# Performance work log

Hardware: AMD Instinct MI355X
Metric: run time of the kernel (lower is better)

Reference implementation:

```python
import jax, jax.numpy as jnp
import numpy as np

N = 1_000_000   # samples
D_IN = 100      # covariate dim (cfg_density[0][0])
H = 64          # hidden dim
NUM_HEADS = 5   # t-bins [0,.2,.4,.6,.8,1.0]


def setup_inputs() -> dict:
    key = jax.random.key(0)
    ks = jax.random.split(key, 17)
    s = 0.05  # param scale for numerical stability (torch init is data-independent anyway)
    return {
        "t": jax.random.uniform(ks[0], (N,), dtype=jnp.float32),
        "x": jax.random.normal(ks[1], (N, D_IN), dtype=jnp.float32),
        # density feature MLP (two Linear+ReLU layers)
        "dW1": jax.random.normal(ks[2], (D_IN, H), dtype=jnp.float32) * s,
        "db1": jax.random.normal(ks[3], (H,), dtype=jnp.float32) * s,
        "dW2": jax.random.normal(ks[4], (H, H), dtype=jnp.float32) * s,
        "db2": jax.random.normal(ks[5], (H,), dtype=jnp.float32) * s,
        # 5 multi-head branches, each 3 Treat_Linear layers (istreat=1 since isenhance=1)
        "hw1": jax.random.normal(ks[6], (NUM_HEADS, H, H), dtype=jnp.float32) * s,
        "htw1": jax.random.normal(ks[7], (NUM_HEADS, H), dtype=jnp.float32) * s,
        "hb1": jax.random.normal(ks[8], (NUM_HEADS, H), dtype=jnp.float32) * s,
        "hw2": jax.random.normal(ks[9], (NUM_HEADS, H, H), dtype=jnp.float32) * s,
        "htw2": jax.random.normal(ks[10], (NUM_HEADS, H), dtype=jnp.float32) * s,
        "hb2": jax.random.normal(ks[11], (NUM_HEADS, H), dtype=jnp.float32) * s,
        "hw3": jax.random.normal(ks[12], (NUM_HEADS, H, 1), dtype=jnp.float32) * s,
        "htw3": jax.random.normal(ks[13], (NUM_HEADS, 1), dtype=jnp.float32) * s,
        "hb3": jax.random.normal(ks[14], (NUM_HEADS, 1), dtype=jnp.float32) * s,
    }


def reference(t, x, dW1, db1, dW2, db2,
              hw1, htw1, hb1, hw2, htw2, hb2, hw3, htw3, hb3):
    # hidden_features: Linear+ReLU, Linear+ReLU
    h = jax.nn.relu(x @ dW1 + db1)        # [N, H]
    h = jax.nn.relu(h @ dW2 + db2)        # [N, H]

    tt = t[:, None]                        # treatment column [N, 1]
    # bin index per row: t in [0.2*q, 0.2*(q+1)); last bin closed at 1.0
    bins = jnp.clip(jnp.floor(t * NUM_HEADS).astype(jnp.int32), 0, NUM_HEADS - 1)

    out = jnp.zeros((x.shape[0], 1), dtype=h.dtype)
    for q in range(NUM_HEADS):  # fixed small set of structurally-distinct heads
        # Treat_Linear layer 1: feat@W + t*tw + b, relu
        a = jax.nn.relu(h @ hw1[q] + tt * htw1[q] + hb1[q])
        # Treat_Linear layer 2
        a = jax.nn.relu(a @ hw2[q] + tt * htw2[q] + hb2[q])
        # last layer: no activation, islastlayer=1
        a = a @ hw3[q] + tt * htw3[q] + hb3[q]   # [N, 1]
        out = out + jnp.where((bins == q)[:, None], a, 0.0)
    return out  # Drnet returns (None, Q); g is None so we return Q
```

## Files before the change

kernel.cpp:

```cpp
#include <hip/hip_runtime.h>

typedef _Float16 f16;
typedef _Float16 f16x8 __attribute__((ext_vector_type(8)));
typedef float f32x16 __attribute__((ext_vector_type(16)));

#define NB 5
#define DIN 100
#define NT 512
#define GRID 256
#define NWAVES (GRID * 8)

#define FID_W2 14
#define FID_HD 22
#define NFID   (FID_HD + NB * 16)
#define NENT   (NFID * 64)

__global__ __launch_bounds__(256)
void prepack_kernel(const float* __restrict__ dW1, const float* __restrict__ dW2,
                    const float* __restrict__ hw1, const float* __restrict__ hw2,
                    f16x8* __restrict__ pw)
{
    int E = blockIdx.x * 256 + threadIdx.x;
    if (E >= NENT) return;
    int lane = E & 63, fid = E >> 6;
    const float* src; int ks, mt, kmax;
    if (fid < FID_W2)      { int f = fid;          ks = f >> 1; mt = f & 1; src = dW1; kmax = 100; }
    else if (fid < FID_HD) { int f = fid - FID_W2; ks = f >> 1; mt = f & 1; src = dW2; kmax = 64; }
    else {
        int f = fid - FID_HD; int q = f >> 4; int r = f & 15;
        int layer = r >> 3; int rr = r & 7; ks = rr >> 1; mt = rr & 1;
        src = (layer ? hw2 : hw1) + q * 4096; kmax = 64;
    }
    f16x8 v;
    #pragma unroll
    for (int e = 0; e < 8; ++e) {
        int k = 16 * ks + 8 * (lane >> 5) + e;
        int m = 32 * mt + (lane & 31);
        v[e] = (k < kmax) ? (f16)src[k * 64 + m] : (f16)0.f;
    }
    pw[E] = v;
}

__device__ __forceinline__ f32x16 mfma32(f16x8 a, f16x8 b, f32x16 c) {
    return __builtin_amdgcn_mfma_f32_32x32x16_f16(a, b, c, 0, 0, 0);
}
__device__ __forceinline__ f32x16 vzero() {
    f32x16 z;
    #pragma unroll
    for (int i = 0; i < 16; ++i) z[i] = 0.f;
    return z;
}
__device__ __forceinline__ unsigned pk2(float a, float b) {
    union { f16 h[2]; unsigned u; } z; z.h[0] = (f16)a; z.h[1] = (f16)b; return z.u;
}
__device__ __forceinline__ f16x8 frag4(unsigned a, unsigned b, unsigned c, unsigned d) {
    union { unsigned u[4]; f16x8 v; } z; z.u[0]=a; z.u[1]=b; z.u[2]=c; z.u[3]=d; return z.v;
}

#define EPI8T(W, A, BIAS, TW, RT, OFF) { \
    const float4* bp_ = (const float4*)((BIAS) + (OFF)); \
    const float4* tp_ = (const float4*)((TW) + (OFF)); \
    float4 b0_=bp_[0], b1_=bp_[2], b2_=bp_[4], b3_=bp_[6]; \
    float4 t0_=tp_[0], t1_=tp_[2], t2_=tp_[4], t3_=tp_[6]; \
    W[0]=pk2(fmaxf(A[0]+b0_.x+(RT)*t0_.x,0.f), fmaxf(A[1]+b0_.y+(RT)*t0_.y,0.f)); \
    W[1]=pk2(fmaxf(A[2]+b0_.z+(RT)*t0_.z,0.f), fmaxf(A[3]+b0_.w+(RT)*t0_.w,0.f)); \
    W[2]=pk2(fmaxf(A[4]+b1_.x+(RT)*t1_.x,0.f), fmaxf(A[5]+b1_.y+(RT)*t1_.y,0.f)); \
    W[3]=pk2(fmaxf(A[6]+b1_.z+(RT)*t1_.z,0.f), fmaxf(A[7]+b1_.w+(RT)*t1_.w,0.f)); \
    W[4]=pk2(fmaxf(A[8]+b2_.x+(RT)*t2_.x,0.f), fmaxf(A[9]+b2_.y+(RT)*t2_.y,0.f)); \
    W[5]=pk2(fmaxf(A[10]+b2_.z+(RT)*t2_.z,0.f), fmaxf(A[11]+b2_.w+(RT)*t2_.w,0.f)); \
    W[6]=pk2(fmaxf(A[12]+b3_.x+(RT)*t3_.x,0.f), fmaxf(A[13]+b3_.y+(RT)*t3_.y,0.f)); \
    W[7]=pk2(fmaxf(A[14]+b3_.z+(RT)*t3_.z,0.f), fmaxf(A[15]+b3_.w+(RT)*t3_.w,0.f)); }

#define EPI8B(W, A, BIAS, OFF) { \
    const float4* bp_ = (const float4*)((BIAS) + (OFF)); \
    float4 b0_=bp_[0], b1_=bp_[2], b2_=bp_[4], b3_=bp_[6]; \
    W[0]=pk2(fmaxf(A[0]+b0_.x,0.f), fmaxf(A[1]+b0_.y,0.f)); \
    W[1]=pk2(fmaxf(A[2]+b0_.z,0.f), fmaxf(A[3]+b0_.w,0.f)); \
    W[2]=pk2(fmaxf(A[4]+b1_.x,0.f), fmaxf(A[5]+b1_.y,0.f)); \
    W[3]=pk2(fmaxf(A[6]+b1_.z,0.f), fmaxf(A[7]+b1_.w,0.f)); \
    W[4]=pk2(fmaxf(A[8]+b2_.x,0.f), fmaxf(A[9]+b2_.y,0.f)); \
    W[5]=pk2(fmaxf(A[10]+b2_.z,0.f), fmaxf(A[11]+b2_.w,0.f)); \
    W[6]=pk2(fmaxf(A[12]+b3_.x,0.f), fmaxf(A[13]+b3_.y,0.f)); \
    W[7]=pk2(fmaxf(A[14]+b3_.z,0.f), fmaxf(A[15]+b3_.w,0.f)); }

#define MKB(dst, Wm, jb) { \
    unsigned s0_=__shfl_xor(Wm[jb+0],32,64), s1_=__shfl_xor(Wm[jb+1],32,64); \
    unsigned s2_=__shfl_xor(Wm[jb+2],32,64), s3_=__shfl_xor(Wm[jb+3],32,64); \
    dst = frag4(lo ? Wm[jb+0] : s2_, lo ? Wm[jb+1] : s3_, \
                lo ? s0_ : Wm[jb+2], lo ? s1_ : Wm[jb+3]); }

#define ACC16(P, A, B2, T2, W3, RT, OFF) { \
    const float4* bb_=(const float4*)((B2)+(OFF)); const float4* tt_=(const float4*)((T2)+(OFF)); \
    const float4* ww_=(const float4*)((W3)+(OFF)); \
    float4 b0_=bb_[0],b1_=bb_[2],b2_=bb_[4],b3_=bb_[6]; \
    float4 t0_=tt_[0],t1_=tt_[2],t2_=tt_[4],t3_=tt_[6]; \
    float4 w0_=ww_[0],w1_=ww_[2],w2_=ww_[4],w3_=ww_[6]; \
    P += fmaxf(A[0]+b0_.x+(RT)*t0_.x,0.f)*w0_.x + fmaxf(A[1]+b0_.y+(RT)*t0_.y,0.f)*w0_.y \
       + fmaxf(A[2]+b0_.z+(RT)*t0_.z,0.f)*w0_.z + fmaxf(A[3]+b0_.w+(RT)*t0_.w,0.f)*w0_.w \
       + fmaxf(A[4]+b1_.x+(RT)*t1_.x,0.f)*w1_.x + fmaxf(A[5]+b1_.y+(RT)*t1_.y,0.f)*w1_.y \
       + fmaxf(A[6]+b1_.z+(RT)*t1_.z,0.f)*w1_.z + fmaxf(A[7]+b1_.w+(RT)*t1_.w,0.f)*w1_.w \
       + fmaxf(A[8]+b2_.x+(RT)*t2_.x,0.f)*w2_.x + fmaxf(A[9]+b2_.y+(RT)*t2_.y,0.f)*w2_.y \
       + fmaxf(A[10]+b2_.z+(RT)*t2_.z,0.f)*w2_.z + fmaxf(A[11]+b2_.w+(RT)*t2_.w,0.f)*w2_.w \
       + fmaxf(A[12]+b3_.x+(RT)*t3_.x,0.f)*w3_.x + fmaxf(A[13]+b3_.y+(RT)*t3_.y,0.f)*w3_.y \
       + fmaxf(A[14]+b3_.z+(RT)*t3_.z,0.f)*w3_.z + fmaxf(A[15]+b3_.w+(RT)*t3_.w,0.f)*w3_.w; }

__global__ __launch_bounds__(NT, 2)
void drnet_main(const float* __restrict__ t, const float* __restrict__ x,
                const float* __restrict__ db1, const float* __restrict__ db2,
                const float* __restrict__ hb1, const float* __restrict__ htw1,
                const float* __restrict__ hb2, const float* __restrict__ htw2,
                const float* __restrict__ hw3, const float* __restrict__ htw3,
                const float* __restrict__ hb3,
                const f16x8* __restrict__ pw,
                float* __restrict__ out, int N, int NG)
{
    __shared__ __align__(16) f16x8 swts[NENT];
    __shared__ __align__(16) float sb1f[64], sb2f[64];
    __shared__ __align__(16) float shb1[NB*64], shw1t[NB*64], shb2[NB*64], shw2t[NB*64], sw3f[NB*64];
    __shared__ float shtw3[NB], shb3[NB];
    __shared__ unsigned short ssrt[8][64];
    __shared__ float sstv[8][64];
    __shared__ float sout[8][64];

    const int tid = threadIdx.x;
    const int lane = tid & 63;
    const int wv = tid >> 6;
    const int hi = lane >> 5;
    const int sm = lane & 31;
    const bool lo = (hi == 0);

    for (int p = tid; p < 64; p += NT) { sb1f[p] = db1[p]; sb2f[p] = db2[p]; }
    for (int p = tid; p < NB*64; p += NT) {
        shb1[p] = hb1[p]; shw1t[p] = htw1[p];
        shb2[p] = hb2[p]; shw2t[p] = htw2[p];
        sw3f[p] = hw3[p];
    }
    if (tid < NB) { shtw3[tid] = htw3[tid]; shb3[tid] = hb3[tid]; }
    for (int p = tid; p < NENT; p += NT)
        ((float4*)swts)[p] = ((const float4*)pw)[p];
    __syncthreads();

    #define TF(fid) swts[(fid)*64 + lane]

    auto do_tile = [&](const f16x8* xb, int li, int rq, float rt, int qlo, int qhiR) {
        if (qlo >= NB) return;
        const int qhi = min(qhiR, NB - 1);

        f32x16 a0 = vzero(), a1 = vzero();
        #pragma unroll
        for (int ks = 0; ks < 7; ++ks) {
            a0 = mfma32(TF(ks*2 + 0), xb[ks], a0);
            a1 = mfma32(TF(ks*2 + 1), xb[ks], a1);
        }
        unsigned WA[8], WB[8];
        EPI8B(WA, a0, sb1f, 4*hi);
        EPI8B(WB, a1, sb1f, 32 + 4*hi);
        f16x8 hb0, hb1_, hb2_, hb3_;
        MKB(hb0, WA, 0); MKB(hb1_, WA, 4); MKB(hb2_, WB, 0); MKB(hb3_, WB, 4);

        f32x16 c0 = vzero(), c1 = vzero();
        c0 = mfma32(TF(FID_W2+0), hb0, c0);  c1 = mfma32(TF(FID_W2+1), hb0, c1);
        c0 = mfma32(TF(FID_W2+2), hb1_, c0); c1 = mfma32(TF(FID_W2+3), hb1_, c1);
        c0 = mfma32(TF(FID_W2+4), hb2_, c0); c1 = mfma32(TF(FID_W2+5), hb2_, c1);
        c0 = mfma32(TF(FID_W2+6), hb3_, c0); c1 = mfma32(TF(FID_W2+7), hb3_, c1);
        unsigned UA[8], UB[8];
        EPI8B(UA, c0, sb2f, 4*hi);
        EPI8B(UB, c1, sb2f, 32 + 4*hi);
        f16x8 g0, g1, g2, g3;
        MKB(g0, UA, 0); MKB(g1, UA, 4); MKB(g2, UB, 0); MKB(g3, UB, 4);

        #pragma unroll 1
        for (int q = qlo; q <= qhi; ++q) {
            const int hf = FID_HD + q * 16;
            f32x16 d0 = vzero(), d1 = vzero();
            d0 = mfma32(TF(hf+0), g0, d0);  d1 = mfma32(TF(hf+1), g0, d1);
            d0 = mfma32(TF(hf+2), g1, d0);  d1 = mfma32(TF(hf+3), g1, d1);
            d0 = mfma32(TF(hf+4), g2, d0);  d1 = mfma32(TF(hf+5), g2, d1);
            d0 = mfma32(TF(hf+6), g3, d0);  d1 = mfma32(TF(hf+7), g3, d1);
            unsigned VA[8], VB[8];
            EPI8T(VA, d0, shb1 + q*64, shw1t + q*64, rt, 4*hi);
            EPI8T(VB, d1, shb1 + q*64, shw1t + q*64, rt, 32 + 4*hi);
            f16x8 e0, e1, e2, e3;
            MKB(e0, VA, 0); MKB(e1, VA, 4); MKB(e2, VB, 0); MKB(e3, VB, 4);

            f32x16 f0 = vzero(), f1 = vzero();
            f0 = mfma32(TF(hf+8),  e0, f0);  f1 = mfma32(TF(hf+9),  e0, f1);
            f0 = mfma32(TF(hf+10), e1, f0);  f1 = mfma32(TF(hf+11), e1, f1);
            f0 = mfma32(TF(hf+12), e2, f0);  f1 = mfma32(TF(hf+13), e2, f1);
            f0 = mfma32(TF(hf+14), e3, f0);  f1 = mfma32(TF(hf+15), e3, f1);

            float part = 0.f;
            ACC16(part, f0, shb2 + q*64, shw2t + q*64, sw3f + q*64, rt, 4*hi);
            ACC16(part, f1, shb2 + q*64, shw2t + q*64, sw3f + q*64, rt, 32 + 4*hi);
            part += __shfl_xor(part, 32, 64);
            if (lo && rq == q)
                sout[wv][li] = part + rt * shtw3[q] + shb3[q];
        }
    };

    auto sortw = [&](int gn, float tvn) {
        const int i0 = gn * 64 + lane;
        const int qme = (i0 < N) ? min((int)(tvn * 5.0f), NB - 1) : NB;
        const unsigned long long lowm = (1ull << lane) - 1ull;
        int pos = 0;
        #pragma unroll
        for (int b = 0; b <= NB; ++b) {
            unsigned long long mb = __ballot(qme == b);
            int ca = __popcll(mb), cb = __popcll(mb & lowm);
            pos += (b < qme) ? ca : ((b == qme) ? cb : 0);
        }
        ssrt[wv][pos] = (unsigned short)(lane | (qme << 8));
        sstv[wv][pos] = tvn;
        __asm__ volatile("s_waitcnt lgkmcnt(0)" ::: "memory");
    };

    auto issue_x = [&](float4* r, int gn, int li) {
        const float4* xp = (const float4*)(x + (size_t)min(gn * 64 + li, N - 1) * DIN);
        #pragma unroll
        for (int ks = 0; ks < 6; ++ks) { r[2*ks] = xp[4*ks + 2*hi]; r[2*ks+1] = xp[4*ks + 2*hi + 1]; }
        r[12] = lo ? xp[24] : make_float4(0.f, 0.f, 0.f, 0.f);
    };

    auto convert = [&](f16x8* xb, const float4* r) {
        #pragma unroll
        for (int ks = 0; ks < 6; ++ks)
            xb[ks] = frag4(pk2(r[2*ks].x, r[2*ks].y),   pk2(r[2*ks].z, r[2*ks].w),
                           pk2(r[2*ks+1].x, r[2*ks+1].y), pk2(r[2*ks+1].z, r[2*ks+1].w));
        xb[6] = frag4(pk2(r[12].x, r[12].y), pk2(r[12].z, r[12].w), 0u, 0u);
    };

    const int gw = blockIdx.x * 8 + wv;
    const int S = NWAVES;

    float4 raw0[13], raw1[13];
    float treg = 0.f;
    int g = gw;
    if (g < NG) {
        treg = t[min(g * 64 + lane, N - 1)];
        sortw(g, treg);
        { int li = ssrt[wv][sm] & 63; issue_x(raw0, g, li); }
        { int gn = g + S; treg = (gn < NG) ? t[min(gn * 64 + lane, N - 1)] : 0.f; }
    }

    #pragma unroll 1
    for (; g < NG; g += S) {
        const unsigned short pk0 = ssrt[wv][sm], pk1 = ssrt[wv][32 + sm];
        const int li0 = pk0 & 63, rq0 = pk0 >> 8;
        const int li1 = pk1 & 63, rq1 = pk1 >> 8;
        const float rt0 = sstv[wv][sm], rt1 = sstv[wv][32 + sm];
        const int qlo0 = ssrt[wv][0]  >> 8, qh0 = ssrt[wv][31] >> 8;
        const int qlo1 = ssrt[wv][32] >> 8, qh1 = ssrt[wv][63] >> 8;

        issue_x(raw1, g, li1);
        f16x8 xb0[7], xb1[7];
        convert(xb0, raw0);
        __builtin_amdgcn_sched_barrier(0);
        do_tile(xb0, li0, rq0, rt0, qlo0, qh0);
        __builtin_amdgcn_sched_barrier(0);

        const bool last = (g + S >= NG);
        if (!last) {
            sortw(g + S, treg);
            { int gn2 = g + 2 * S; treg = (gn2 < NG) ? t[min(gn2 * 64 + lane, N - 1)] : 0.f; }
            { int li = ssrt[wv][sm] & 63; issue_x(raw0, g + S, li); }
            __builtin_amdgcn_sched_barrier(0);
        }
        convert(xb1, raw1);
        do_tile(xb1, li1, rq1, rt1, qlo1, qh1);

        __asm__ volatile("s_waitcnt lgkmcnt(0)" ::: "memory");
        const int ig = g * 64 + lane;
        if (ig < N) out[ig] = sout[wv][lane];
    }
    #undef TF
}

extern "C" void kernel_launch(void* const* d_in, const int* in_sizes, int n_in,
                              void* d_out, int out_size, void* d_ws, size_t ws_size,
                              hipStream_t stream) {
    const float* t    = (const float*)d_in[0];
    const float* x    = (const float*)d_in[1];
    const float* dW1  = (const float*)d_in[2];
    const float* db1  = (const float*)d_in[3];
    const float* dW2  = (const float*)d_in[4];
    const float* db2  = (const float*)d_in[5];
    const float* hw1  = (const float*)d_in[6];
    const float* htw1 = (const float*)d_in[7];
    const float* hb1  = (const float*)d_in[8];
    const float* hw2  = (const float*)d_in[9];
    const float* htw2 = (const float*)d_in[10];
    const float* hb2  = (const float*)d_in[11];
    const float* hw3  = (const float*)d_in[12];
    const float* htw3 = (const float*)d_in[13];
    const float* hb3  = (const float*)d_in[14];
    float* out = (float*)d_out;

    const int N = in_sizes[0];
    const int NG = (N + 63) / 64;
    f16x8* pw = (f16x8*)d_ws;

    prepack_kernel<<<(NENT + 255) / 256, 256, 0, stream>>>(dW1, dW2, hw1, hw2, pw);
    drnet_main<<<GRID, NT, 0, stream>>>(t, x, db1, db2, hb1, htw1, hb2, htw2,
                                        hw3, htw3, hb3, pw, out, N, NG);
}
```

Baseline: 150.6 us.

## Fold biases, treatment terms and final layer into extra MFMA K-steps

```diff
diff --git a/kernel.cpp b/kernel.cpp
--- a/kernel.cpp
+++ b/kernel.cpp
@@ -3,6 +3,7 @@
 typedef _Float16 f16;
 typedef _Float16 f16x8 __attribute__((ext_vector_type(8)));
 typedef float f32x16 __attribute__((ext_vector_type(16)));
+typedef unsigned long long u64;
 
 #define NB 5
 #define DIN 100
@@ -11,32 +12,68 @@
 #define NWAVES (GRID * 8)
 
 #define FID_W2 14
-#define FID_HD 22
-#define NFID   (FID_HD + NB * 16)
+#define FID_HD 24
+#define NFID   (FID_HD + NB * 25)
 #define NENT   (NFID * 64)
 
 __global__ __launch_bounds__(256)
-void prepack_kernel(const float* __restrict__ dW1, const float* __restrict__ dW2,
-                    const float* __restrict__ hw1, const float* __restrict__ hw2,
+void prepack_kernel(const float* __restrict__ dW1, const float* __restrict__ db1,
+                    const float* __restrict__ dW2, const float* __restrict__ db2,
+                    const float* __restrict__ hw1, const float* __restrict__ htw1, const float* __restrict__ hb1,
+                    const float* __restrict__ hw2, const float* __restrict__ htw2, const float* __restrict__ hb2,
+                    const float* __restrict__ hw3, const float* __restrict__ htw3, const float* __restrict__ hb3,
                     f16x8* __restrict__ pw)
 {
     int E = blockIdx.x * 256 + threadIdx.x;
     if (E >= NENT) return;
-    int lane = E & 63, fid = E >> 6;
-    const float* src; int ks, mt, kmax;
-    if (fid < FID_W2)      { int f = fid;          ks = f >> 1; mt = f & 1; src = dW1; kmax = 100; }
-    else if (fid < FID_HD) { int f = fid - FID_W2; ks = f >> 1; mt = f & 1; src = dW2; kmax = 64; }
-    else {
-        int f = fid - FID_HD; int q = f >> 4; int r = f & 15;
-        int layer = r >> 3; int rr = r & 7; ks = rr >> 1; mt = rr & 1;
-        src = (layer ? hw2 : hw1) + q * 4096; kmax = 64;
-    }
+    const int lane = E & 63, fid = E >> 6;
+    const int hi8 = (lane >> 5) * 8, m = lane & 31;
     f16x8 v;
-    #pragma unroll
-    for (int e = 0; e < 8; ++e) {
-        int k = 16 * ks + 8 * (lane >> 5) + e;
-        int m = 32 * mt + (lane & 31);
-        v[e] = (k < kmax) ? (f16)src[k * 64 + m] : (f16)0.f;
+    if (fid < FID_W2) {
+        int ks = fid >> 1, mm = (fid & 1) * 32 + m;
+        #pragma unroll
+        for (int e = 0; e < 8; ++e) {
+            int k = 16 * ks + hi8 + e;
+            float val = (k < 100) ? dW1[k * 64 + mm] : (k == 100 ? db1[mm] : 0.f);
+            v[e] = (f16)val;
+        }
+    } else if (fid < FID_HD) {
+        int f = fid - FID_W2;
+        int ks = f >> 1, mm = (f & 1) * 32 + m;
+        #pragma unroll
+        for (int e = 0; e < 8; ++e) {
+            int k = 16 * ks + hi8 + e;
+            float val = (k < 64) ? dW2[k * 64 + mm] : (k == 64 ? db2[mm] : 0.f);
+            v[e] = (f16)val;
+        }
+    } else {
+        int f = fid - FID_HD, q = f / 25, r = f % 25;
+        if (r < 20) {
+            int layer = r / 10, rr = r % 10;
+            int ks = rr >> 1, mm = (rr & 1) * 32 + m;
+            const float* W = layer ? hw2 : hw1;
+            const float* B = layer ? hb2 : hb1;
+            const float* T = layer ? htw2 : htw1;
+            #pragma unroll
+            for (int e = 0; e < 8; ++e) {
+                int k = 16 * ks + hi8 + e;
+                float val = (k < 64) ? W[q * 4096 + k * 64 + mm]
+                          : (k == 64 ? B[q * 64 + mm]
+                          : (k == 65 ? T[q * 64 + mm] : 0.f));
+                v[e] = (f16)val;
+            }
+        } else {
+            int ks = r - 20;
+            #pragma unroll
+            for (int e = 0; e < 8; ++e) {
+                int k = 16 * ks + hi8 + e;
+                float val = 0.f;
+                if (m == 0)
+                    val = (k < 64) ? hw3[q * 64 + k]
+                        : (k == 64 ? hb3[q] : (k == 65 ? htw3[q] : 0.f));
+                v[e] = (f16)val;
+            }
+        }
     }
     pw[E] = v;
 }
@@ -57,31 +94,15 @@
     union { unsigned u[4]; f16x8 v; } z; z.u[0]=a; z.u[1]=b; z.u[2]=c; z.u[3]=d; return z.v;
 }
 
-#define EPI8T(W, A, BIAS, TW, RT, OFF) { \
-    const float4* bp_ = (const float4*)((BIAS) + (OFF)); \
-    const float4* tp_ = (const float4*)((TW) + (OFF)); \
-    float4 b0_=bp_[0], b1_=bp_[2], b2_=bp_[4], b3_=bp_[6]; \
-    float4 t0_=tp_[0], t1_=tp_[2], t2_=tp_[4], t3_=tp_[6]; \
-    W[0]=pk2(fmaxf(A[0]+b0_.x+(RT)*t0_.x,0.f), fmaxf(A[1]+b0_.y+(RT)*t0_.y,0.f)); \
-    W[1]=pk2(fmaxf(A[2]+b0_.z+(RT)*t0_.z,0.f), fmaxf(A[3]+b0_.w+(RT)*t0_.w,0.f)); \
-    W[2]=pk2(fmaxf(A[4]+b1_.x+(RT)*t1_.x,0.f), fmaxf(A[5]+b1_.y+(RT)*t1_.y,0.f)); \
-    W[3]=pk2(fmaxf(A[6]+b1_.z+(RT)*t1_.z,0.f), fmaxf(A[7]+b1_.w+(RT)*t1_.w,0.f)); \
-    W[4]=pk2(fmaxf(A[8]+b2_.x+(RT)*t2_.x,0.f), fmaxf(A[9]+b2_.y+(RT)*t2_.y,0.f)); \
-    W[5]=pk2(fmaxf(A[10]+b2_.z+(RT)*t2_.z,0.f), fmaxf(A[11]+b2_.w+(RT)*t2_.w,0.f)); \
-    W[6]=pk2(fmaxf(A[12]+b3_.x+(RT)*t3_.x,0.f), fmaxf(A[13]+b3_.y+(RT)*t3_.y,0.f)); \
-    W[7]=pk2(fmaxf(A[14]+b3_.z+(RT)*t3_.z,0.f), fmaxf(A[15]+b3_.w+(RT)*t3_.w,0.f)); }
-
-#define EPI8B(W, A, BIAS, OFF) { \
-    const float4* bp_ = (const float4*)((BIAS) + (OFF)); \
-    float4 b0_=bp_[0], b1_=bp_[2], b2_=bp_[4], b3_=bp_[6]; \
-    W[0]=pk2(fmaxf(A[0]+b0_.x,0.f), fmaxf(A[1]+b0_.y,0.f)); \
-    W[1]=pk2(fmaxf(A[2]+b0_.z,0.f), fmaxf(A[3]+b0_.w,0.f)); \
-    W[2]=pk2(fmaxf(A[4]+b1_.x,0.f), fmaxf(A[5]+b1_.y,0.f)); \
-    W[3]=pk2(fmaxf(A[6]+b1_.z,0.f), fmaxf(A[7]+b1_.w,0.f)); \
-    W[4]=pk2(fmaxf(A[8]+b2_.x,0.f), fmaxf(A[9]+b2_.y,0.f)); \
-    W[5]=pk2(fmaxf(A[10]+b2_.z,0.f), fmaxf(A[11]+b2_.w,0.f)); \
-    W[6]=pk2(fmaxf(A[12]+b3_.x,0.f), fmaxf(A[13]+b3_.y,0.f)); \
-    W[7]=pk2(fmaxf(A[14]+b3_.z,0.f), fmaxf(A[15]+b3_.w,0.f)); }
+#define EPIR(W, A) { \
+    W[0]=pk2(fmaxf(A[0],0.f), fmaxf(A[1],0.f)); \
+    W[1]=pk2(fmaxf(A[2],0.f), fmaxf(A[3],0.f)); \
+    W[2]=pk2(fmaxf(A[4],0.f), fmaxf(A[5],0.f)); \
+    W[3]=pk2(fmaxf(A[6],0.f), fmaxf(A[7],0.f)); \
+    W[4]=pk2(fmaxf(A[8],0.f), fmaxf(A[9],0.f)); \
+    W[5]=pk2(fmaxf(A[10],0.f),fmaxf(A[11],0.f)); \
+    W[6]=pk2(fmaxf(A[12],0.f),fmaxf(A[13],0.f)); \
+    W[7]=pk2(fmaxf(A[14],0.f),fmaxf(A[15],0.f)); }
 
 #define MKB(dst, Wm, jb) { \
     unsigned s0_=__shfl_xor(Wm[jb+0],32,64), s1_=__shfl_xor(Wm[jb+1],32,64); \
@@ -89,35 +110,12 @@
     dst = frag4(lo ? Wm[jb+0] : s2_, lo ? Wm[jb+1] : s3_, \
                 lo ? s0_ : Wm[jb+2], lo ? s1_ : Wm[jb+3]); }
 
-#define ACC16(P, A, B2, T2, W3, RT, OFF) { \
-    const float4* bb_=(const float4*)((B2)+(OFF)); const float4* tt_=(const float4*)((T2)+(OFF)); \
-    const float4* ww_=(const float4*)((W3)+(OFF)); \
-    float4 b0_=bb_[0],b1_=bb_[2],b2_=bb_[4],b3_=bb_[6]; \
-    float4 t0_=tt_[0],t1_=tt_[2],t2_=tt_[4],t3_=tt_[6]; \
-    float4 w0_=ww_[0],w1_=ww_[2],w2_=ww_[4],w3_=ww_[6]; \
-    P += fmaxf(A[0]+b0_.x+(RT)*t0_.x,0.f)*w0_.x + fmaxf(A[1]+b0_.y+(RT)*t0_.y,0.f)*w0_.y \
-       + fmaxf(A[2]+b0_.z+(RT)*t0_.z,0.f)*w0_.z + fmaxf(A[3]+b0_.w+(RT)*t0_.w,0.f)*w0_.w \
-       + fmaxf(A[4]+b1_.x+(RT)*t1_.x,0.f)*w1_.x + fmaxf(A[5]+b1_.y+(RT)*t1_.y,0.f)*w1_.y \
-       + fmaxf(A[6]+b1_.z+(RT)*t1_.z,0.f)*w1_.z + fmaxf(A[7]+b1_.w+(RT)*t1_.w,0.f)*w1_.w \
-       + fmaxf(A[8]+b2_.x+(RT)*t2_.x,0.f)*w2_.x + fmaxf(A[9]+b2_.y+(RT)*t2_.y,0.f)*w2_.y \
-       + fmaxf(A[10]+b2_.z+(RT)*t2_.z,0.f)*w2_.z + fmaxf(A[11]+b2_.w+(RT)*t2_.w,0.f)*w2_.w \
-       + fmaxf(A[12]+b3_.x+(RT)*t3_.x,0.f)*w3_.x + fmaxf(A[13]+b3_.y+(RT)*t3_.y,0.f)*w3_.y \
-       + fmaxf(A[14]+b3_.z+(RT)*t3_.z,0.f)*w3_.z + fmaxf(A[15]+b3_.w+(RT)*t3_.w,0.f)*w3_.w; }
-
 __global__ __launch_bounds__(NT, 2)
 void drnet_main(const float* __restrict__ t, const float* __restrict__ x,
-                const float* __restrict__ db1, const float* __restrict__ db2,
-                const float* __restrict__ hb1, const float* __restrict__ htw1,
-                const float* __restrict__ hb2, const float* __restrict__ htw2,
-                const float* __restrict__ hw3, const float* __restrict__ htw3,
-                const float* __restrict__ hb3,
                 const f16x8* __restrict__ pw,
                 float* __restrict__ out, int N, int NG)
 {
     __shared__ __align__(16) f16x8 swts[NENT];
-    __shared__ __align__(16) float sb1f[64], sb2f[64];
-    __shared__ __align__(16) float shb1[NB*64], shw1t[NB*64], shb2[NB*64], shw2t[NB*64], sw3f[NB*64];
-    __shared__ float shtw3[NB], shb3[NB];
     __shared__ unsigned short ssrt[8][64];
     __shared__ float sstv[8][64];
     __shared__ float sout[8][64];
@@ -129,20 +127,15 @@
     const int sm = lane & 31;
     const bool lo = (hi == 0);
 
-    for (int p = tid; p < 64; p += NT) { sb1f[p] = db1[p]; sb2f[p] = db2[p]; }
-    for (int p = tid; p < NB*64; p += NT) {
-        shb1[p] = hb1[p]; shw1t[p] = htw1[p];
-        shb2[p] = hb2[p]; shw2t[p] = htw2[p];
-        sw3f[p] = hw3[p];
-    }
-    if (tid < NB) { shtw3[tid] = htw3[tid]; shb3[tid] = hb3[tid]; }
     for (int p = tid; p < NENT; p += NT)
         ((float4*)swts)[p] = ((const float4*)pw)[p];
     __syncthreads();
 
     #define TF(fid) swts[(fid)*64 + lane]
 
-    auto do_tile = [&](const f16x8* xb, int li, int rq, float rt, int qlo, int qhiR) {
+    const f16x8 bfb = lo ? frag4(pk2(1.f, 0.f), 0u, 0u, 0u) : frag4(0u, 0u, 0u, 0u);
+
+    auto do_tile = [&](const f16x8* xb, f16x8 bft, int li, int rq, int qlo, int qhiR) {
         if (qlo >= NB) return;
         const int qhi = min(qhiR, NB - 1);
 
@@ -153,59 +146,65 @@
             a1 = mfma32(TF(ks*2 + 1), xb[ks], a1);
         }
         unsigned WA[8], WB[8];
-        EPI8B(WA, a0, sb1f, 4*hi);
-        EPI8B(WB, a1, sb1f, 32 + 4*hi);
-        f16x8 hb0, hb1_, hb2_, hb3_;
-        MKB(hb0, WA, 0); MKB(hb1_, WA, 4); MKB(hb2_, WB, 0); MKB(hb3_, WB, 4);
+        EPIR(WA, a0); EPIR(WB, a1);
+        f16x8 h0, h1_, h2_, h3_;
+        MKB(h0, WA, 0); MKB(h1_, WA, 4); MKB(h2_, WB, 0); MKB(h3_, WB, 4);
 
         f32x16 c0 = vzero(), c1 = vzero();
-        c0 = mfma32(TF(FID_W2+0), hb0, c0);  c1 = mfma32(TF(FID_W2+1), hb0, c1);
-        c0 = mfma32(TF(FID_W2+2), hb1_, c0); c1 = mfma32(TF(FID_W2+3), hb1_, c1);
-        c0 = mfma32(TF(FID_W2+4), hb2_, c0); c1 = mfma32(TF(FID_W2+5), hb2_, c1);
-        c0 = mfma32(TF(FID_W2+6), hb3_, c0); c1 = mfma32(TF(FID_W2+7), hb3_, c1);
+        c0 = mfma32(TF(FID_W2+0), h0, c0);  c1 = mfma32(TF(FID_W2+1), h0, c1);
+        c0 = mfma32(TF(FID_W2+2), h1_, c0); c1 = mfma32(TF(FID_W2+3), h1_, c1);
+        c0 = mfma32(TF(FID_W2+4), h2_, c0); c1 = mfma32(TF(FID_W2+5), h2_, c1);
+        c0 = mfma32(TF(FID_W2+6), h3_, c0); c1 = mfma32(TF(FID_W2+7), h3_, c1);
+        c0 = mfma32(TF(FID_W2+8), bfb, c0); c1 = mfma32(TF(FID_W2+9), bfb, c1);
         unsigned UA[8], UB[8];
-        EPI8B(UA, c0, sb2f, 4*hi);
-        EPI8B(UB, c1, sb2f, 32 + 4*hi);
+        EPIR(UA, c0); EPIR(UB, c1);
         f16x8 g0, g1, g2, g3;
         MKB(g0, UA, 0); MKB(g1, UA, 4); MKB(g2, UB, 0); MKB(g3, UB, 4);
 
         #pragma unroll 1
         for (int q = qlo; q <= qhi; ++q) {
-            const int hf = FID_HD + q * 16;
+            const int hf = FID_HD + q * 25;
             f32x16 d0 = vzero(), d1 = vzero();
             d0 = mfma32(TF(hf+0), g0, d0);  d1 = mfma32(TF(hf+1), g0, d1);
             d0 = mfma32(TF(hf+2), g1, d0);  d1 = mfma32(TF(hf+3), g1, d1);
             d0 = mfma32(TF(hf+4), g2, d0);  d1 = mfma32(TF(hf+5), g2, d1);
             d0 = mfma32(TF(hf+6), g3, d0);  d1 = mfma32(TF(hf+7), g3, d1);
+            d0 = mfma32(TF(hf+8), bft, d0); d1 = mfma32(TF(hf+9), bft, d1);
             unsigned VA[8], VB[8];
-            EPI8T(VA, d0, shb1 + q*64, shw1t + q*64, rt, 4*hi);
-            EPI8T(VB, d1, shb1 + q*64, shw1t + q*64, rt, 32 + 4*hi);
+            EPIR(VA, d0); EPIR(VB, d1);
             f16x8 e0, e1, e2, e3;
             MKB(e0, VA, 0); MKB(e1, VA, 4); MKB(e2, VB, 0); MKB(e3, VB, 4);
 
             f32x16 f0 = vzero(), f1 = vzero();
-            f0 = mfma32(TF(hf+8),  e0, f0);  f1 = mfma32(TF(hf+9),  e0, f1);
-            f0 = mfma32(TF(hf+10), e1, f0);  f1 = mfma32(TF(hf+11), e1, f1);
-            f0 = mfma32(TF(hf+12), e2, f0);  f1 = mfma32(TF(hf+13), e2, f1);
-            f0 = mfma32(TF(hf+14), e3, f0);  f1 = mfma32(TF(hf+15), e3, f1);
-
-            float part = 0.f;
-            ACC16(part, f0, shb2 + q*64, shw2t + q*64, sw3f + q*64, rt, 4*hi);
-            ACC16(part, f1, shb2 + q*64, shw2t + q*64, sw3f + q*64, rt, 32 + 4*hi);
-            part += __shfl_xor(part, 32, 64);
+            f0 = mfma32(TF(hf+10), e0, f0);  f1 = mfma32(TF(hf+11), e0, f1);
+            f0 = mfma32(TF(hf+12), e1, f0);  f1 = mfma32(TF(hf+13), e1, f1);
+            f0 = mfma32(TF(hf+14), e2, f0);  f1 = mfma32(TF(hf+15), e2, f1);
+            f0 = mfma32(TF(hf+16), e3, f0);  f1 = mfma32(TF(hf+17), e3, f1);
+            f0 = mfma32(TF(hf+18), bft, f0); f1 = mfma32(TF(hf+19), bft, f1);
+            unsigned YA[8], YB[8];
+            EPIR(YA, f0); EPIR(YB, f1);
+            f16x8 z0, z1, z2, z3;
+            MKB(z0, YA, 0); MKB(z1, YA, 4); MKB(z2, YB, 0); MKB(z3, YB, 4);
+
+            f32x16 o0 = vzero();
+            o0 = mfma32(TF(hf+20), z0, o0);
+            o0 = mfma32(TF(hf+21), z1, o0);
+            o0 = mfma32(TF(hf+22), z2, o0);
+            o0 = mfma32(TF(hf+23), z3, o0);
+            o0 = mfma32(TF(hf+24), bft, o0);
             if (lo && rq == q)
-                sout[wv][li] = part + rt * shtw3[q] + shb3[q];
+                sout[wv][li] = o0[0];
         }
     };
 
     auto sortw = [&](int gn, float tvn) {
         const int i0 = gn * 64 + lane;
         const int qme = (i0 < N) ? min((int)(tvn * 5.0f), NB - 1) : NB;
-        const unsigned long long lowm = (1ull << lane) - 1ull;
+        const u64 lowm = (1ull << lane) - 1ull;
         int pos = 0;
         #pragma unroll
         for (int b = 0; b <= NB; ++b) {
-            unsigned long long mb = __ballot(qme == b);
+            u64 mb = __ballot(qme == b);
             int ca = __popcll(mb), cb = __popcll(mb & lowm);
             pos += (b < qme) ? ca : ((b == qme) ? cb : 0);
         }
@@ -226,7 +225,8 @@
         for (int ks = 0; ks < 6; ++ks)
             xb[ks] = frag4(pk2(r[2*ks].x, r[2*ks].y),   pk2(r[2*ks].z, r[2*ks].w),
                            pk2(r[2*ks+1].x, r[2*ks+1].y), pk2(r[2*ks+1].z, r[2*ks+1].w));
-        xb[6] = frag4(pk2(r[12].x, r[12].y), pk2(r[12].z, r[12].w), 0u, 0u);
+        xb[6] = frag4(pk2(r[12].x, r[12].y), pk2(r[12].z, r[12].w),
+                      lo ? pk2(1.0f, 0.f) : 0u, 0u);
     };
 
     const int gw = blockIdx.x * 8 + wv;
@@ -250,12 +250,14 @@
         const float rt0 = sstv[wv][sm], rt1 = sstv[wv][32 + sm];
         const int qlo0 = ssrt[wv][0]  >> 8, qh0 = ssrt[wv][31] >> 8;
         const int qlo1 = ssrt[wv][32] >> 8, qh1 = ssrt[wv][63] >> 8;
+        const f16x8 bft0 = lo ? frag4(pk2(1.f, rt0), 0u, 0u, 0u) : frag4(0u, 0u, 0u, 0u);
+        const f16x8 bft1 = lo ? frag4(pk2(1.f, rt1), 0u, 0u, 0u) : frag4(0u, 0u, 0u, 0u);
 
         issue_x(raw1, g, li1);
         f16x8 xb0[7], xb1[7];
         convert(xb0, raw0);
         __builtin_amdgcn_sched_barrier(0);
-        do_tile(xb0, li0, rq0, rt0, qlo0, qh0);
+        do_tile(xb0, bft0, li0, rq0, qlo0, qh0);
         __builtin_amdgcn_sched_barrier(0);
 
         const bool last = (g + S >= NG);
@@ -266,7 +268,7 @@
             __builtin_amdgcn_sched_barrier(0);
         }
         convert(xb1, raw1);
-        do_tile(xb1, li1, rq1, rt1, qlo1, qh1);
+        do_tile(xb1, bft1, li1, rq1, qlo1, qh1);
 
         __asm__ volatile("s_waitcnt lgkmcnt(0)" ::: "memory");
         const int ig = g * 64 + lane;
@@ -299,7 +301,7 @@
     const int NG = (N + 63) / 64;
     f16x8* pw = (f16x8*)d_ws;
 
-    prepack_kernel<<<(NENT + 255) / 256, 256, 0, stream>>>(dW1, dW2, hw1, hw2, pw);
-    drnet_main<<<GRID, NT, 0, stream>>>(t, x, db1, db2, hb1, htw1, hb2, htw2,
-                                        hw3, htw3, hb3, pw, out, N, NG);
-}
+    prepack_kernel<<<(NENT + 255) / 256, 256, 0, stream>>>(
+        dW1, db1, dW2, db2, hw1, htw1, hb1, hw2, htw2, hb2, hw3, htw3, hb3, pw);
+    drnet_main<<<GRID, NT, 0, stream>>>(t, x, pw, out, N, NG);
+}
```

Result: no change. 151.4 us (+0.5%).
